# Optimization experiments

Measured on AMD Instinct MI355X. Metric: run time of the kernel, lower is better.

The kernel has to match this reference:

```python
import jax, jax.numpy as jnp
import numpy as np

N = 100000
E = 640000
D = 128
L = 3
B = 128
OUT = 10


def setup_inputs() -> dict:
    key = jax.random.key(0)
    ks = jax.random.split(key, 8)
    x = jax.random.normal(ks[0], (N, D), dtype=jnp.float32)
    edge_index = jax.random.randint(ks[1], (2, E), 0, N, dtype=jnp.int64)
    batch = jnp.sort(jax.random.randint(ks[2], (N,), 0, B, dtype=jnp.int64))
    # per-layer GCNConv weights (in==hidden==D so they stack) and biases
    Ws = jax.random.normal(ks[3], (L, D, D), dtype=jnp.float32) / np.sqrt(D)
    bs = jnp.zeros((L, D), dtype=jnp.float32)
    # MLP head: single Linear(hidden -> out), norm=None
    W_mlp = jax.random.normal(ks[4], (D, OUT), dtype=jnp.float32) / np.sqrt(D)
    b_mlp = jnp.zeros((OUT,), dtype=jnp.float32)
    return {"x": x, "edge_index": edge_index, "batch": batch,
            "Ws": Ws, "bs": bs, "W_mlp": W_mlp, "b_mlp": b_mlp}


def reference(x, edge_index, batch, Ws, bs, W_mlp, b_mlp):
    n = x.shape[0]
    # --- GCN normalization (PyG gcn_norm with self-loops, edge_weight=1) ---
    loop = jnp.arange(n, dtype=edge_index.dtype)
    src = jnp.concatenate([edge_index[0], loop])  # message sources (x_j)
    dst = jnp.concatenate([edge_index[1], loop])  # aggregation targets
    deg = jax.ops.segment_sum(jnp.ones_like(dst, dtype=x.dtype), dst, num_segments=n)
    dinv = jnp.where(deg > 0, jax.lax.rsqrt(jnp.maximum(deg, 1.0)), 0.0)
    norm = dinv[src] * dinv[dst]  # [E+N]

    def gcn_conv(h, W, b):
        hw = h @ W  # [N, D] dense transform
        msg = hw[src] * norm[:, None]  # gather + scale [E+N, D]
        agg = jax.ops.segment_sum(msg, dst, num_segments=n)  # scatter-add
        return agg + b

    h = x
    for l in range(Ws.shape[0]):
        h = jax.nn.relu(gcn_conv(h, Ws[l], bs[l]))

    # global add pool over graphs
    pooled = jax.ops.segment_sum(h, batch, num_segments=B)  # [B, D]
    # MLP head (single linear, no norm/act)
    return pooled @ W_mlp + b_mlp
```

## Files before the change

kernel.cpp:

```cpp
#include <hip/hip_runtime.h>
#include <hip/hip_bf16.h>

#define N_NODES 100000
#define N_EDGES 640000
#define DIM 128
#define N_LAYERS 3
#define N_GRAPHS 128
#define N_OUT 10
#define SCAN_BLK 1024
#define N_SCAN_BLKS ((N_NODES + SCAN_BLK - 1) / SCAN_BLK)
#define PCHUNK 128
#define NXCD 8
#define RNODES (N_NODES / NXCD)
#define R_EST 98304
#define BE 1000
#define RK 40

typedef _Float16 h4 __attribute__((ext_vector_type(4)));
typedef _Float16 h2 __attribute__((ext_vector_type(2)));
typedef _Float16 h8 __attribute__((ext_vector_type(8)));
typedef float f32x4 __attribute__((ext_vector_type(4)));


__global__ __launch_bounds__(256) void bucket_edges(const int* __restrict__ ei,
                                                    int* __restrict__ rangeCur,
                                                    int2* __restrict__ staging) {
    __shared__ int hist[NXCD];
    __shared__ int base[NXCD];
    const int e0 = blockIdx.x * BE;
    if (threadIdx.x < NXCD) hist[threadIdx.x] = 0;
    __syncthreads();

    int s[4], d[4], r[4];
    #pragma unroll
    for (int k = 0; k < 4; ++k) {
        int e = e0 + threadIdx.x + k * 256;
        if (e < e0 + BE) {
            s[k] = ei[e];
            d[k] = ei[N_EDGES + e];
            r[k] = d[k] / RNODES;
            atomicAdd(&hist[r[k]], 1);
        } else r[k] = -1;
    }
    __syncthreads();
    if (threadIdx.x < NXCD) base[threadIdx.x] = atomicAdd(&rangeCur[threadIdx.x], hist[threadIdx.x]);
    __syncthreads();
    if (threadIdx.x < NXCD) hist[threadIdx.x] = 0;
    __syncthreads();

    #pragma unroll
    for (int k = 0; k < 4; ++k) {
        if (r[k] >= 0) {
            int idx = base[r[k]] + atomicAdd(&hist[r[k]], 1);
            staging[(size_t)r[k] * R_EST + idx] = make_int2(s[k], d[k]);
        }
    }
}


__global__ __launch_bounds__(256) void hist_pinned(const int2* __restrict__ staging,
                                                   const int* __restrict__ rangeCur,
                                                   int* __restrict__ cnt) {
    const int g = blockIdx.x & (NXCD - 1);
    const int b = blockIdx.x >> 3;
    const int n = rangeCur[g];
    const int2* st = staging + (size_t)g * R_EST;
    for (int j = b * 256 + threadIdx.x; j < n; j += RK * 256)
        atomicAdd(&cnt[st[j].y], 1);
}


__global__ void scan1(const int* __restrict__ cnt, int* __restrict__ off, int* __restrict__ bsum,
                      float* __restrict__ dinv) {
    __shared__ int tmp[256];
    int base = blockIdx.x * SCAN_BLK + threadIdx.x * 4;
    int c[4];
    #pragma unroll
    for (int k = 0; k < 4; ++k) c[k] = (base + k < N_NODES) ? cnt[base + k] : 0;
    #pragma unroll
    for (int k = 0; k < 4; ++k)
        if (base + k < N_NODES) dinv[base + k] = rsqrtf((float)(c[k] + 1));
    int tot = c[0] + c[1] + c[2] + c[3];
    tmp[threadIdx.x] = tot;
    __syncthreads();
    int val = tot;
    for (int d = 1; d < 256; d <<= 1) {
        int add = (threadIdx.x >= d) ? tmp[threadIdx.x - d] : 0;
        __syncthreads();
        val += add;
        tmp[threadIdx.x] = val;
        __syncthreads();
    }
    int ex = val - tot;
    int e1 = ex + c[0], e2 = e1 + c[1], e3 = e2 + c[2];
    if (base + 0 < N_NODES) off[base + 0] = ex;
    if (base + 1 < N_NODES) off[base + 1] = e1;
    if (base + 2 < N_NODES) off[base + 2] = e2;
    if (base + 3 < N_NODES) off[base + 3] = e3;
    if (threadIdx.x == 255) bsum[blockIdx.x] = val;
}

__global__ void scan2(int* __restrict__ bsum) {
    __shared__ int tmp[128];
    int t = threadIdx.x;
    int v = (t < N_SCAN_BLKS) ? bsum[t] : 0;
    int own = v;
    tmp[t] = v;
    __syncthreads();
    for (int d = 1; d < 128; d <<= 1) {
        int add = (t >= d) ? tmp[t - d] : 0;
        __syncthreads();
        v += add;
        tmp[t] = v;
        __syncthreads();
    }
    if (t < N_SCAN_BLKS) bsum[t] = v - own;
}

__global__ void scan3(int* __restrict__ off, const int* __restrict__ bsum) {
    int i = blockIdx.x * blockDim.x + threadIdx.x;
    if (i < N_NODES) off[i] += bsum[i / SCAN_BLK];
    if (i == 0) off[N_NODES] = N_EDGES;
}


__global__ __launch_bounds__(256) void fill_pinned(const int2* __restrict__ staging,
                                                   const int* __restrict__ rangeCur,
                                                   const int* __restrict__ off,
                                                   int* __restrict__ cursor,
                                                   int* __restrict__ csr_src) {
    const int g = blockIdx.x & (NXCD - 1);
    const int b = blockIdx.x >> 3;
    const int n = rangeCur[g];
    const int2* st = staging + (size_t)g * R_EST;
    for (int j = b * 256 + threadIdx.x; j < n; j += RK * 256) {
        int2 sd = st[j];
        int pos = off[sd.y] + atomicAdd(&cursor[sd.y], 1);
        csr_src[pos] = sd.x;
    }
}


__global__ void wt_prep(const float* __restrict__ Ws, _Float16* __restrict__ wt) {
    int t = blockIdx.x * blockDim.x + threadIdx.x;
    if (t >= N_LAYERS * DIM * 32) return;
    int u = t & 31;
    int n = (t >> 5) & 127;
    int l = t >> 12;
    const float* W = Ws + (size_t)l * DIM * DIM;
    int k0 = u * 4;
    h4 v;
    v.x = (_Float16)W[(k0 + 0) * DIM + n];
    v.y = (_Float16)W[(k0 + 1) * DIM + n];
    v.z = (_Float16)W[(k0 + 2) * DIM + n];
    v.w = (_Float16)W[(k0 + 3) * DIM + n];
    int du = u ^ (n & 31);
    ((h4*)wt)[(size_t)l * 4096 + n * 32 + du] = v;
}


__device__ __forceinline__ h4 loadfrag(const _Float16* p) { return *(const h4*)p; }
__device__ __forceinline__ h4 loadfrag(const float* p) {
    float4 f = *(const float4*)p;
    h4 v; v.x = (_Float16)f.x; v.y = (_Float16)f.y; v.z = (_Float16)f.z; v.w = (_Float16)f.w;
    return v;
}

template<typename TIN>
__global__ __launch_bounds__(256) void gemm_mfma(const TIN* __restrict__ in,
                                                 const _Float16* __restrict__ wt,
                                                 const float* __restrict__ dinv,
                                                 _Float16* __restrict__ out) {
    __shared__ h4 Wl[4096];
    {
        const float4* src = (const float4*)wt;
        float4* dst = (float4*)Wl;
        #pragma unroll
        for (int i = 0; i < 8; ++i) dst[threadIdx.x + i * 256] = src[threadIdx.x + i * 256];
    }
    __syncthreads();

    const int wave = threadIdx.x >> 6;
    const int lane = threadIdx.x & 63;
    const int m0 = blockIdx.x * 64 + wave * 16;
    if (m0 >= N_NODES) return;

    const int row = lane & 15;
    const int g   = lane >> 4;
    const int m   = m0 + row;
    const TIN* arow = in + (size_t)m * DIM;
    const float di = dinv[m];

    f32x4 acc[8] = {};

    #pragma unroll
    for (int kc = 0; kc < 8; ++kc) {
        const int k = kc * 16 + g * 4;
        const h4 bfrag = loadfrag(arow + k);
        const int u = kc * 4 + g;
        #pragma unroll
        for (int nb = 0; nb < 8; ++nb) {
            const int n = nb * 16 + row;
            const h4 afrag = Wl[n * 32 + (u ^ (n & 31))];
            acc[nb] = __builtin_amdgcn_mfma_f32_16x16x16f16(afrag, bfrag, acc[nb], 0, 0, 0);
        }
    }

    _Float16* orow = out + (size_t)m * DIM;
    #pragma unroll
    for (int nb = 0; nb < 8; ++nb) {
        h4 v;
        v.x = (_Float16)(acc[nb].x * di); v.y = (_Float16)(acc[nb].y * di);
        v.z = (_Float16)(acc[nb].z * di); v.w = (_Float16)(acc[nb].w * di);
        ((h4*)orow)[nb * 4 + g] = v;
    }
}


__global__ __launch_bounds__(256) void gather_agg(const _Float16* __restrict__ hw,
                                                  const float* __restrict__ dinv,
                                                  const int* __restrict__ off,
                                                  const int* __restrict__ csr_src,
                                                  const float* __restrict__ bias,
                                                  _Float16* __restrict__ hout) {
    const int i = (blockIdx.x * blockDim.x + threadIdx.x) >> 6;
    if (i >= N_NODES) return;
    const int lane = threadIdx.x & 63;
    const int grp    = lane >> 3;
    const int stream = grp & 3;
    const int half   = grp >> 2;
    const int sub    = lane & 7;
    const int idx8   = half * 8 + sub;
    const h8* hw8 = (const h8*)hw;

    const int beg = off[i], end = off[i + 1];
    h8 acc = {};

    if (stream == 3) acc = hw8[(size_t)i * 16 + idx8];

    int j = beg + stream;
    for (; j + 4 < end; j += 8) {
        int s0 = csr_src[j];
        int s1 = csr_src[j + 4];
        h8 v0 = hw8[(size_t)s0 * 16 + idx8];
        h8 v1 = hw8[(size_t)s1 * 16 + idx8];
        #pragma unroll
        for (int p = 0; p < 4; ++p) {
            ((h2*)&acc)[p] += ((h2*)&v0)[p];
            ((h2*)&acc)[p] += ((h2*)&v1)[p];
        }
    }
    for (; j < end; j += 4) {
        int s0 = csr_src[j];
        h8 v0 = hw8[(size_t)s0 * 16 + idx8];
        #pragma unroll
        for (int p = 0; p < 4; ++p) ((h2*)&acc)[p] += ((h2*)&v0)[p];
    }

    unsigned int* au = (unsigned int*)&acc;
    #pragma unroll
    for (int p = 0; p < 4; ++p) {
        unsigned int o = __shfl_xor(au[p], 8);
        h2 a = *(h2*)&au[p]; a += *(h2*)&o; au[p] = *(unsigned int*)&a;
        o = __shfl_xor(au[p], 16);
        h2 b = *(h2*)&au[p]; b += *(h2*)&o; au[p] = *(unsigned int*)&b;
    }

    if (stream == 0) {
        const float di = dinv[i];
        const float4 b0 = *(const float4*)&bias[half * 64 + sub * 8];
        const float4 b1 = *(const float4*)&bias[half * 64 + sub * 8 + 4];
        h8 v;
        v[0] = (_Float16)fmaxf((float)acc[0] * di + b0.x, 0.0f);
        v[1] = (_Float16)fmaxf((float)acc[1] * di + b0.y, 0.0f);
        v[2] = (_Float16)fmaxf((float)acc[2] * di + b0.z, 0.0f);
        v[3] = (_Float16)fmaxf((float)acc[3] * di + b0.w, 0.0f);
        v[4] = (_Float16)fmaxf((float)acc[4] * di + b1.x, 0.0f);
        v[5] = (_Float16)fmaxf((float)acc[5] * di + b1.y, 0.0f);
        v[6] = (_Float16)fmaxf((float)acc[6] * di + b1.z, 0.0f);
        v[7] = (_Float16)fmaxf((float)acc[7] * di + b1.w, 0.0f);
        ((h8*)hout)[(size_t)i * 16 + idx8] = v;
    }
}


__global__ __launch_bounds__(256) void pool_chunk(const _Float16* __restrict__ h,
                                                  const int* __restrict__ batch,
                                                  float* __restrict__ pooled) {
    const int base = blockIdx.x * PCHUNK;
    const int t = threadIdx.x;
    const int lane4 = t & 31;
    const int rgrp = t >> 5;
    const h4* hp = (const h4*)h;

    float a0 = 0.f, a1 = 0.f, a2 = 0.f, a3 = 0.f;
    int cur = -1;
    const int rend = (base + PCHUNK < N_NODES) ? base + PCHUNK : N_NODES;
    for (int r = base + rgrp; r < rend; r += 8) {
        int b = batch[r];
        if (b != cur) {
            if (cur >= 0) {
                float* pp = &pooled[cur * DIM + lane4 * 4];
                atomicAdd(pp + 0, a0); atomicAdd(pp + 1, a1);
                atomicAdd(pp + 2, a2); atomicAdd(pp + 3, a3);
            }
            cur = b; a0 = a1 = a2 = a3 = 0.f;
        }
        h4 v = hp[(size_t)r * 32 + lane4];
        a0 += (float)v.x; a1 += (float)v.y; a2 += (float)v.z; a3 += (float)v.w;
    }
    if (cur >= 0) {
        float* pp = &pooled[cur * DIM + lane4 * 4];
        atomicAdd(pp + 0, a0); atomicAdd(pp + 1, a1);
        atomicAdd(pp + 2, a2); atomicAdd(pp + 3, a3);
    }
}


__global__ void mlp_head(const float* __restrict__ pooled, const float* __restrict__ Wm,
                         const float* __restrict__ bm, float* __restrict__ out) {
    int t = blockIdx.x * blockDim.x + threadIdx.x;
    if (t >= N_GRAPHS * N_OUT) return;
    int b = t / N_OUT;
    int o = t % N_OUT;
    float acc = bm[o];
    #pragma unroll 8
    for (int k = 0; k < DIM; ++k) acc += pooled[b * DIM + k] * Wm[k * N_OUT + o];
    out[t] = acc;
}


extern "C" void kernel_launch(void* const* d_in, const int* in_sizes, int n_in,
                              void* d_out, int out_size, void* d_ws, size_t ws_size,
                              hipStream_t stream) {
    const float* x     = (const float*)d_in[0];
    const int*   ei    = (const int*)d_in[1];
    const int*   batch = (const int*)d_in[2];
    const float* Ws    = (const float*)d_in[3];
    const float* bs    = (const float*)d_in[4];
    const float* Wm    = (const float*)d_in[5];
    const float* bm    = (const float*)d_in[6];
    float* out = (float*)d_out;

    char* p = (char*)d_ws;
    int*      cnt      = (int*)p;        p += N_NODES * 4;
    int*      cursor   = (int*)p;        p += N_NODES * 4;
    int*      rangeCur = (int*)p;        p += 16 * 4;
    float*    dinv     = (float*)p;      p += N_NODES * 4;
    int*      csr_off  = (int*)p;        p += (N_NODES + 16) * 4;
    int*      bsum     = (int*)p;        p += 128 * 4;
    _Float16* wt       = (_Float16*)p;   p += (size_t)N_LAYERS * DIM * DIM * 2;
    int*      csr_src  = (int*)p;        p += (size_t)N_EDGES * 4;
    int2*     staging  = (int2*)p;       p += (size_t)NXCD * R_EST * 8;
    _Float16* bufA     = (_Float16*)p;   p += (size_t)N_NODES * DIM * 2;
    _Float16* bufB     = (_Float16*)p;   p += (size_t)N_NODES * DIM * 2;
    float*    pooled   = (float*)p;      p += N_GRAPHS * DIM * 4;

    const int nnode_blk = (N_NODES + 255) / 256;

    hipMemsetAsync(cnt, 0, N_NODES * 8 + 16 * 4, stream);
    hipMemsetAsync(pooled, 0, N_GRAPHS * DIM * 4, stream);

    bucket_edges<<<N_EDGES / BE, 256, 0, stream>>>(ei, rangeCur, staging);
    wt_prep<<<(N_LAYERS * DIM * 32 + 255) / 256, 256, 0, stream>>>(Ws, wt);

    hist_pinned<<<NXCD * RK, 256, 0, stream>>>(staging, rangeCur, cnt);

    scan1<<<N_SCAN_BLKS, 256, 0, stream>>>(cnt, csr_off, bsum, dinv);
    scan2<<<1, 128, 0, stream>>>(bsum);
    scan3<<<nnode_blk, 256, 0, stream>>>(csr_off, bsum);

    fill_pinned<<<NXCD * RK, 256, 0, stream>>>(staging, rangeCur, csr_off, cursor, csr_src);

    const int gemm_grid = (N_NODES + 63) / 64;
    const int gather_grid = (N_NODES * 64 + 255) / 256;
    for (int l = 0; l < N_LAYERS; ++l) {
        if (l == 0) gemm_mfma<float><<<gemm_grid, 256, 0, stream>>>(x, wt, dinv, bufA);
        else        gemm_mfma<_Float16><<<gemm_grid, 256, 0, stream>>>(bufB, wt + (size_t)l * DIM * DIM, dinv, bufA);
        gather_agg<<<gather_grid, 256, 0, stream>>>(bufA, dinv, csr_off, csr_src, bs + l * DIM, bufB);
    }

    pool_chunk<<<(N_NODES + PCHUNK - 1) / PCHUNK, 256, 0, stream>>>(bufB, batch, pooled);
    mlp_head<<<(N_GRAPHS * N_OUT + 255) / 256, 256, 0, stream>>>(pooled, Wm, bm, out);
}
```

Measured before the change: 290.2 us.

## Make GEMM persistent with register double-buffered prefetch of next row tile

The MFMA GEMM kernel now launches a fixed grid of 512 blocks that loop over row tiles in grid-stride fashion, instead of one block per 64 rows. Each wave prefetches the next tile's A fragments and dinv into registers while it computes the current tile, so global-load latency overlaps the MFMA work. This also amortizes the per-block LDS load of the weight matrix across many tiles. In exchange it raises register pressure, and with fewer blocks occupancy and latency hiding between waves may drop.

```diff
diff --git a/kernel.cpp b/kernel.cpp
--- a/kernel.cpp
+++ b/kernel.cpp
@@ -15,6 +15,7 @@
 #define R_EST 98304
 #define BE 1000
 #define RK 40
+#define GEMM_GRID 512
 
 typedef _Float16 h4 __attribute__((ext_vector_type(4)));
 typedef _Float16 h2 __attribute__((ext_vector_type(2)));
@@ -182,37 +183,67 @@
 
     const int wave = threadIdx.x >> 6;
     const int lane = threadIdx.x & 63;
-    const int m0 = blockIdx.x * 64 + wave * 16;
-    if (m0 >= N_NODES) return;
-
     const int row = lane & 15;
     const int g   = lane >> 4;
-    const int m   = m0 + row;
-    const TIN* arow = in + (size_t)m * DIM;
-    const float di = dinv[m];
-
-    f32x4 acc[8] = {};
-
-    #pragma unroll
-    for (int kc = 0; kc < 8; ++kc) {
-        const int k = kc * 16 + g * 4;
-        const h4 bfrag = loadfrag(arow + k);
-        const int u = kc * 4 + g;
+    const int STEP = GEMM_GRID * 64;
+
+    int c0 = blockIdx.x * 64;
+    h4 bf[8];
+    float di = 0.f;
+    bool valid = false;
+    {
+        int m0 = c0 + wave * 16;
+        if (c0 < N_NODES && m0 < N_NODES) {
+            valid = true;
+            const TIN* ar = in + (size_t)(m0 + row) * DIM;
+            di = dinv[m0 + row];
+            #pragma unroll
+            for (int kc = 0; kc < 8; ++kc) bf[kc] = loadfrag(ar + kc * 16 + g * 4);
+        }
+    }
+
+    for (; c0 < N_NODES; c0 += STEP) {
+        const int c1 = c0 + STEP;
+        h4 bf2[8];
+        float di2 = 0.f;
+        bool valid2 = false;
+        if (c1 < N_NODES) {
+            int m1 = c1 + wave * 16;
+            if (m1 < N_NODES) {
+                valid2 = true;
+                const TIN* ar2 = in + (size_t)(m1 + row) * DIM;
+                di2 = dinv[m1 + row];
+                #pragma unroll
+                for (int kc = 0; kc < 8; ++kc) bf2[kc] = loadfrag(ar2 + kc * 16 + g * 4);
+            }
+        }
+
+        if (valid) {
+            f32x4 acc[8] = {};
+            #pragma unroll
+            for (int kc = 0; kc < 8; ++kc) {
+                const int u = kc * 4 + g;
+                #pragma unroll
+                for (int nb = 0; nb < 8; ++nb) {
+                    const int n = nb * 16 + row;
+                    const h4 afrag = Wl[n * 32 + (u ^ (n & 31))];
+                    acc[nb] = __builtin_amdgcn_mfma_f32_16x16x16f16(afrag, bf[kc], acc[nb], 0, 0, 0);
+                }
+            }
+            _Float16* orow = out + (size_t)(c0 + wave * 16 + row) * DIM;
+            #pragma unroll
+            for (int nb = 0; nb < 8; ++nb) {
+                h4 v;
+                v.x = (_Float16)(acc[nb].x * di); v.y = (_Float16)(acc[nb].y * di);
+                v.z = (_Float16)(acc[nb].z * di); v.w = (_Float16)(acc[nb].w * di);
+                ((h4*)orow)[nb * 4 + g] = v;
+            }
+        }
+
         #pragma unroll
-        for (int nb = 0; nb < 8; ++nb) {
-            const int n = nb * 16 + row;
-            const h4 afrag = Wl[n * 32 + (u ^ (n & 31))];
-            acc[nb] = __builtin_amdgcn_mfma_f32_16x16x16f16(afrag, bfrag, acc[nb], 0, 0, 0);
-        }
-    }
-
-    _Float16* orow = out + (size_t)m * DIM;
-    #pragma unroll
-    for (int nb = 0; nb < 8; ++nb) {
-        h4 v;
-        v.x = (_Float16)(acc[nb].x * di); v.y = (_Float16)(acc[nb].y * di);
-        v.z = (_Float16)(acc[nb].z * di); v.w = (_Float16)(acc[nb].w * di);
-        ((h4*)orow)[nb * 4 + g] = v;
+        for (int kc = 0; kc < 8; ++kc) bf[kc] = bf2[kc];
+        di = di2;
+        valid = valid2;
     }
 }
 
@@ -372,11 +403,10 @@
 
     fill_pinned<<<NXCD * RK, 256, 0, stream>>>(staging, rangeCur, csr_off, cursor, csr_src);
 
-    const int gemm_grid = (N_NODES + 63) / 64;
     const int gather_grid = (N_NODES * 64 + 255) / 256;
     for (int l = 0; l < N_LAYERS; ++l) {
-        if (l == 0) gemm_mfma<float><<<gemm_grid, 256, 0, stream>>>(x, wt, dinv, bufA);
-        else        gemm_mfma<_Float16><<<gemm_grid, 256, 0, stream>>>(bufB, wt + (size_t)l * DIM * DIM, dinv, bufA);
+        if (l == 0) gemm_mfma<float><<<GEMM_GRID, 256, 0, stream>>>(x, wt, dinv, bufA);
+        else        gemm_mfma<_Float16><<<GEMM_GRID, 256, 0, stream>>>(bufB, wt + (size_t)l * DIM * DIM, dinv, bufA);
         gather_agg<<<gather_grid, 256, 0, stream>>>(bufA, dinv, csr_off, csr_src, bs + l * DIM, bufB);
     }
 
```

After: 286.1 us. About the same (-1.4%).
